# Kernel tuning notes

Hardware: AMD Instinct MI355X
Metric: run time of the kernel (lower is better)

## Reference

```python
import jax, jax.numpy as jnp
import numpy as np
from jax import lax

IMSIZE = 4096
LINEWIDTH = 31  # odd, matches torch init adjustment


def _gen_kernel(lw):
    # Nested concentric squares: layer i covers [i, lw-i) with value (i+1)/(center+1);
    # inner layers overwrite outer ones, so value = (center - chebyshev_r + 1)/(center+1).
    c = lw // 2
    idx = jnp.arange(lw)
    r = jnp.maximum(jnp.abs(idx[:, None] - c), jnp.abs(idx[None, :] - c))
    val = (c - r + 1).astype(jnp.float32) / jnp.float32(c + 1)
    return jnp.broadcast_to(val, (3, 3, lw, lw))


def _rasterize(x0, y0, x1, y1, imsize):
    # Faithful port of the torch Bresenham variant (including the inner while loop).
    # All coordinate math is non-differentiable in the original (done via .data),
    # so we stop gradients here.
    x0 = lax.stop_gradient(x0)
    y0 = lax.stop_gradient(y0)
    x1 = lax.stop_gradient(x1)
    y1 = lax.stop_gradient(y1)
    dx = jnp.abs(x1 - x0)
    dy = jnp.abs(y1 - y0)
    sx = jnp.where(x1 > x0, 1.0, -1.0)
    sy = jnp.where(y1 > y0, 1.0, -1.0)
    steep = dy > dx
    # swap (x0,y0), (dx,dy), (sx,sy) when steep
    a = jnp.where(steep, y0, x0)
    b = jnp.where(steep, x0, y0)
    dX = jnp.where(steep, dy, dx)
    dY = jnp.where(steep, dx, dy)
    sa = jnp.where(steep, sy, sx)
    sb = jnp.where(steep, sx, sy)
    d = 2.0 * dY - dX
    n = dX.astype(jnp.int32)
    mask0 = jnp.zeros((imsize, imsize), dtype=jnp.float32)

    def body(i, carry):
        a, b, d, mask = carry
        row = jnp.where(steep, b, a).astype(jnp.int32)
        col = jnp.where(steep, a, b).astype(jnp.int32)
        mask = mask.at[row, col].set(1.0)

        def inner(bd):
            bb, dd = bd
            return (bb + sb, dd - 2.0 * dX)

        b, d = lax.while_loop(lambda bd: bd[1] >= 0.0, inner, (b, d))
        a = a + sa
        d = d + 2.0 * dY
        return (a, b, d, mask)

    _, _, _, mask = lax.fori_loop(0, n, body, (a, b, d, mask0))
    mask = mask.at[x1.astype(jnp.int32), y1.astype(jnp.int32)].set(1.0)
    return mask


def setup_inputs() -> dict:
    return {
        "x0": jnp.array([100.0], dtype=jnp.float32),
        "y0": jnp.array([200.0], dtype=jnp.float32),
        "x1": jnp.array([3900.0], dtype=jnp.float32),
        "y1": jnp.array([3500.0], dtype=jnp.float32),
    }


def reference(x0, y0, x1, y1):
    imsize, lw = IMSIZE, LINEWIDTH
    mask = _rasterize(x0[0], y0[0], x1[0], y1[0], imsize)  # [H, W]
    img = jnp.broadcast_to(mask, (1, 3, imsize, imsize))   # NCHW
    kernel = _gen_kernel(lw)                               # OIHW [3,3,lw,lw]
    pad = lw // 2
    out = lax.conv_general_dilated(
        img, kernel, window_strides=(1, 1),
        padding=[(pad, pad), (pad, pad)],
        dimension_numbers=("NCHW", "OIHW", "NCHW"))
    tmin = jnp.min(out)
    tmax = jnp.max(out)
    out = (out - tmin) / (tmax - tmin)
    return 1.0 - out[0]  # [3, imsize, imsize]
```

## Files before the change

### kernel.cpp

```cpp
#include <hip/hip_runtime.h>
#include <cstdint>
#include <cstddef>

#define IMSIZE 4096
#define HALF 15
#define SENT (-100000)

__global__ __launch_bounds__(1024) void k_line(
    const float* __restrict__ x0p, const float* __restrict__ y0p,
    const float* __restrict__ x1p, const float* __restrict__ y1p,
    int* __restrict__ hdr, int* __restrict__ map)
{
    int t = threadIdx.x;
    for (int i = t; i < IMSIZE; i += 1024) map[i] = SENT;
    __syncthreads();

    float x0 = x0p[0], y0 = y0p[0], x1 = x1p[0], y1 = y1p[0];
    float dx = fabsf(x1 - x0), dy = fabsf(y1 - y0);
    float sx = (x1 > x0) ? 1.f : -1.f;
    float sy = (y1 > y0) ? 1.f : -1.f;
    bool steep = dy > dx;
    float a0 = steep ? y0 : x0;
    float b0 = steep ? x0 : y0;
    float dX = steep ? dy : dx;
    float dY = steep ? dx : dy;
    float sa = steep ? sy : sx;
    float sb = steep ? sx : sy;
    int n = (int)dX;

    if (t == 0) { hdr[0] = steep ? 1 : 0; hdr[1] = 0; }

    double twodY = 2.0 * (double)dY;
    double twodX = 2.0 * (double)dX;
    double ddX   = (double)dX;
    for (int i = t; i < n; i += 1024) {
        int ki = (int)floor((twodY * (double)i + ddX) / twodX);
        float ai = a0 + sa * (float)i;
        float bi = b0 + sb * (float)ki;
        int M  = (int)ai;
        int mn = (int)bi;
        if ((unsigned)M < IMSIZE) map[M] = mn;
    }
    if (t == 0) {
        int M  = steep ? (int)y1 : (int)x1;
        int mn = steep ? (int)x1 : (int)y1;
        if ((unsigned)M < IMSIZE) map[M] = mn;
    }
}

__device__ __forceinline__ int conv_s(int i, int j, int steep,
                                      const int* __restrict__ map)
{
    int M  = steep ? j : i;
    int mn = steep ? i : j;
    int s = 0;
    #pragma unroll
    for (int dm = -HALF; dm <= HALF; ++dm) {
        int m = M + dm;
        if ((unsigned)m < IMSIZE) {
            int c = map[m];
            int ad = abs(c - mn);
            if (ad <= HALF) s += 16 - max(ad, (dm < 0 ? -dm : dm));
        }
    }
    return s;
}

__global__ __launch_bounds__(64) void k_band(
    int* __restrict__ hdr, const int* __restrict__ map,
    int* __restrict__ lo, int* __restrict__ hi)
{
    int M = blockIdx.x;
    int t = threadIdx.x;

    int v = SENT;
    if (t < 2 * HALF + 1) {
        int m = M - HALF + t;
        if ((unsigned)m < IMSIZE) v = map[m];
    }
    int vmin = (v <= SENT / 2) ? 0x7fffffff : v;
    int vmax = (v <= SENT / 2) ? (-0x7fffffff - 1) : v;
    #pragma unroll
    for (int o = 32; o >= 1; o >>= 1) {
        vmin = min(vmin, __shfl_xor(vmin, o));
        vmax = max(vmax, __shfl_xor(vmax, o));
    }
    int L, H;
    if (vmin == 0x7fffffff) { L = 1; H = 0; }
    else { L = max(vmin - HALF, 0); H = min(vmax + HALF, IMSIZE - 1); }
    if (t == 0) { lo[M] = L; hi[M] = H; }

    int steep = hdr[0];
    int smax = 0;
    for (int j = L + t; j <= H; j += 64) {
        int row = steep ? j : M;
        int col = steep ? M : j;
        smax = max(smax, conv_s(row, col, steep, map));
    }
    #pragma unroll
    for (int o = 32; o >= 1; o >>= 1) smax = max(smax, __shfl_xor(smax, o));
    if (t == 0 && smax > 0) atomicMax(hdr + 1, smax);
}

__global__ __launch_bounds__(256) void k_fill(float4* __restrict__ out)
{
    size_t idx = (size_t)blockIdx.x * 256 + threadIdx.x;
    out[idx] = make_float4(1.f, 1.f, 1.f, 1.f);
}

__global__ __launch_bounds__(64) void k_patch(
    const int* __restrict__ hdr, const int* __restrict__ map,
    const int* __restrict__ lo, const int* __restrict__ hi,
    float* __restrict__ out)
{
    int M = blockIdx.x;
    int t = threadIdx.x;
    int L = lo[M], H = hi[M];
    int steep = hdr[0];
    float inv = 1.0f / (float)hdr[1];
    const size_t CH = (size_t)IMSIZE * IMSIZE;

    for (int j = L + t; j <= H; j += 64) {
        int row = steep ? j : M;
        int col = steep ? M : j;
        int s = conv_s(row, col, steep, map);
        float val = 1.0f - (float)s * inv;
        size_t p = (size_t)row * IMSIZE + col;
        out[p]          = val;
        out[p + CH]     = val;
        out[p + 2 * CH] = val;
    }
}

extern "C" void kernel_launch(void* const* d_in, const int* in_sizes, int n_in,
                              void* d_out, int out_size, void* d_ws, size_t ws_size,
                              hipStream_t stream)
{
    const float* x0 = (const float*)d_in[0];
    const float* y0 = (const float*)d_in[1];
    const float* x1 = (const float*)d_in[2];
    const float* y1 = (const float*)d_in[3];

    int* ws  = (int*)d_ws;
    int* hdr = ws;
    int* map = ws + 16;
    int* lo  = ws + 16 + IMSIZE;
    int* hi  = ws + 16 + 2 * IMSIZE;
    float* out = (float*)d_out;

    const int NF4 = 3 * IMSIZE * IMSIZE / 4;

    hipLaunchKernelGGL(k_fill,  dim3(NF4 / 256), dim3(256),  0, stream,
                       (float4*)out);
    hipLaunchKernelGGL(k_line,  dim3(1),         dim3(1024), 0, stream,
                       x0, y0, x1, y1, hdr, map);
    hipLaunchKernelGGL(k_band,  dim3(IMSIZE),    dim3(64),   0, stream,
                       hdr, map, lo, hi);
    hipLaunchKernelGGL(k_patch, dim3(IMSIZE),    dim3(64),   0, stream,
                       hdr, map, lo, hi, out);
}
```

Baseline: 250.7 us.

## Compute line map analytically per row, drop line/band kernels and workspace map

Removes the single-block line rasterization kernel and the global map/lo/hi arrays. Each row block now recomputes its 31-entry window of the Bresenham map analytically into shared memory and derives the band bounds itself, in both the max pass and the patch pass. The fill kernel becomes grid-stride with fewer blocks and also resets the max header. This cuts one serial launch and the global-memory round trips, at the cost of redundant per-block double-precision division work.

```diff
diff --git a/kernel.cpp b/kernel.cpp
--- a/kernel.cpp
+++ b/kernel.cpp
@@ -5,126 +5,131 @@
 #define IMSIZE 4096
 #define HALF 15
 #define SENT (-100000)
+#define INT_MAXV 0x7fffffff
+#define INT_MINV (-0x7fffffff - 1)
 
-__global__ __launch_bounds__(1024) void k_line(
+struct LineP {
+    int steep, saPos, Mbase, n, Mend, mnend;
+    float b0, sb;
+    double twodY, twodX, ddX;
+};
+
+__device__ __forceinline__ LineP line_params(
     const float* __restrict__ x0p, const float* __restrict__ y0p,
-    const float* __restrict__ x1p, const float* __restrict__ y1p,
-    int* __restrict__ hdr, int* __restrict__ map)
+    const float* __restrict__ x1p, const float* __restrict__ y1p)
 {
-    int t = threadIdx.x;
-    for (int i = t; i < IMSIZE; i += 1024) map[i] = SENT;
-    __syncthreads();
-
     float x0 = x0p[0], y0 = y0p[0], x1 = x1p[0], y1 = y1p[0];
     float dx = fabsf(x1 - x0), dy = fabsf(y1 - y0);
     float sx = (x1 > x0) ? 1.f : -1.f;
     float sy = (y1 > y0) ? 1.f : -1.f;
-    bool steep = dy > dx;
-    float a0 = steep ? y0 : x0;
-    float b0 = steep ? x0 : y0;
-    float dX = steep ? dy : dx;
-    float dY = steep ? dx : dy;
-    float sa = steep ? sy : sx;
-    float sb = steep ? sx : sy;
-    int n = (int)dX;
-
-    if (t == 0) { hdr[0] = steep ? 1 : 0; hdr[1] = 0; }
-
-    double twodY = 2.0 * (double)dY;
-    double twodX = 2.0 * (double)dX;
-    double ddX   = (double)dX;
-    for (int i = t; i < n; i += 1024) {
-        int ki = (int)floor((twodY * (double)i + ddX) / twodX);
-        float ai = a0 + sa * (float)i;
-        float bi = b0 + sb * (float)ki;
-        int M  = (int)ai;
-        int mn = (int)bi;
-        if ((unsigned)M < IMSIZE) map[M] = mn;
-    }
-    if (t == 0) {
-        int M  = steep ? (int)y1 : (int)x1;
-        int mn = steep ? (int)x1 : (int)y1;
-        if ((unsigned)M < IMSIZE) map[M] = mn;
-    }
+    LineP P;
+    P.steep = dy > dx;
+    float a0 = P.steep ? y0 : x0;
+    float dX = P.steep ? dy : dx;
+    float dY = P.steep ? dx : dy;
+    float sa = P.steep ? sy : sx;
+    P.b0 = P.steep ? x0 : y0;
+    P.sb = P.steep ? sx : sy;
+    P.saPos = sa > 0.f;
+    P.Mbase = (int)a0;
+    P.n     = (int)dX;
+    P.Mend  = P.steep ? (int)y1 : (int)x1;
+    P.mnend = P.steep ? (int)x1 : (int)y1;
+    P.twodY = 2.0 * (double)dY;
+    P.twodX = 2.0 * (double)dX;
+    P.ddX   = (double)dX;
+    return P;
 }
 
-__device__ __forceinline__ int conv_s(int i, int j, int steep,
-                                      const int* __restrict__ map)
+__device__ __forceinline__ int map_at(const LineP& P, int m)
 {
-    int M  = steep ? j : i;
-    int mn = steep ? i : j;
-    int s = 0;
-    #pragma unroll
-    for (int dm = -HALF; dm <= HALF; ++dm) {
-        int m = M + dm;
-        if ((unsigned)m < IMSIZE) {
-            int c = map[m];
-            int ad = abs(c - mn);
-            if (ad <= HALF) s += 16 - max(ad, (dm < 0 ? -dm : dm));
-        }
-    }
-    return s;
+    if ((unsigned)m >= IMSIZE) return SENT;
+    if (m == P.Mend) return P.mnend;
+    int i = P.saPos ? (m - P.Mbase) : (P.Mbase - m);
+    if (i < 0 || i >= P.n) return SENT;
+    int ki = (int)floor((P.twodY * (double)i + P.ddX) / P.twodX);
+    float bi = P.b0 + P.sb * (float)ki;
+    return (int)bi;
 }
 
-__global__ __launch_bounds__(64) void k_band(
-    int* __restrict__ hdr, const int* __restrict__ map,
-    int* __restrict__ lo, int* __restrict__ hi)
+__device__ __forceinline__ void band_window(
+    const LineP& P, int M, int t, int* wmap, int& L, int& H)
 {
-    int M = blockIdx.x;
-    int t = threadIdx.x;
-
-    int v = SENT;
-    if (t < 2 * HALF + 1) {
-        int m = M - HALF + t;
-        if ((unsigned)m < IMSIZE) v = map[m];
-    }
-    int vmin = (v <= SENT / 2) ? 0x7fffffff : v;
-    int vmax = (v <= SENT / 2) ? (-0x7fffffff - 1) : v;
+    if (t < 2 * HALF + 1) wmap[t] = map_at(P, M - HALF + t);
+    __syncthreads();
+    int v = (t < 2 * HALF + 1) ? wmap[t] : SENT;
+    int vmin = (v <= SENT / 2) ? INT_MAXV : v;
+    int vmax = (v <= SENT / 2) ? INT_MINV : v;
     #pragma unroll
     for (int o = 32; o >= 1; o >>= 1) {
         vmin = min(vmin, __shfl_xor(vmin, o));
         vmax = max(vmax, __shfl_xor(vmax, o));
     }
+    if (vmin == INT_MAXV) { L = 1; H = 0; }
+    else { L = max(vmin - HALF, 0); H = min(vmax + HALF, IMSIZE - 1); }
+}
+
+__device__ __forceinline__ int conv_w(const int* __restrict__ wmap, int j)
+{
+    int s = 0;
+    #pragma unroll
+    for (int dm = -HALF; dm <= HALF; ++dm) {
+        int c = wmap[dm + HALF];
+        int ad = abs(c - j);
+        if (ad <= HALF) s += 16 - max(ad, (dm < 0 ? -dm : dm));
+    }
+    return s;
+}
+
+__global__ __launch_bounds__(256) void k_fill(float4* __restrict__ out,
+                                              int* __restrict__ hdr)
+{
+    if (blockIdx.x == 0 && threadIdx.x == 0) hdr[1] = 0;
+    const size_t N4 = (size_t)3 * IMSIZE * IMSIZE / 4;
+    size_t stride = (size_t)gridDim.x * 256;
+    const float4 one = make_float4(1.f, 1.f, 1.f, 1.f);
+    for (size_t i = (size_t)blockIdx.x * 256 + threadIdx.x; i < N4; i += stride)
+        out[i] = one;
+}
+
+__global__ __launch_bounds__(64) void k_smax(
+    const float* __restrict__ x0p, const float* __restrict__ y0p,
+    const float* __restrict__ x1p, const float* __restrict__ y1p,
+    int* __restrict__ hdr)
+{
+    __shared__ int wmap[32];
+    LineP P = line_params(x0p, y0p, x1p, y1p);
+    int M = blockIdx.x, t = threadIdx.x;
     int L, H;
-    if (vmin == 0x7fffffff) { L = 1; H = 0; }
-    else { L = max(vmin - HALF, 0); H = min(vmax + HALF, IMSIZE - 1); }
-    if (t == 0) { lo[M] = L; hi[M] = H; }
+    band_window(P, M, t, wmap, L, H);
 
-    int steep = hdr[0];
     int smax = 0;
-    for (int j = L + t; j <= H; j += 64) {
-        int row = steep ? j : M;
-        int col = steep ? M : j;
-        smax = max(smax, conv_s(row, col, steep, map));
-    }
+    for (int j = L + t; j <= H; j += 64)
+        smax = max(smax, conv_w(wmap, j));
     #pragma unroll
     for (int o = 32; o >= 1; o >>= 1) smax = max(smax, __shfl_xor(smax, o));
-    if (t == 0 && smax > 0) atomicMax(hdr + 1, smax);
-}
-
-__global__ __launch_bounds__(256) void k_fill(float4* __restrict__ out)
-{
-    size_t idx = (size_t)blockIdx.x * 256 + threadIdx.x;
-    out[idx] = make_float4(1.f, 1.f, 1.f, 1.f);
+    if (t == 0) atomicMax(hdr + 1, smax);
 }
 
 __global__ __launch_bounds__(64) void k_patch(
-    const int* __restrict__ hdr, const int* __restrict__ map,
-    const int* __restrict__ lo, const int* __restrict__ hi,
-    float* __restrict__ out)
+    const float* __restrict__ x0p, const float* __restrict__ y0p,
+    const float* __restrict__ x1p, const float* __restrict__ y1p,
+    const int* __restrict__ hdr, float* __restrict__ out)
 {
-    int M = blockIdx.x;
-    int t = threadIdx.x;
-    int L = lo[M], H = hi[M];
-    int steep = hdr[0];
+    __shared__ int wmap[32];
+    LineP P = line_params(x0p, y0p, x1p, y1p);
+    int M = blockIdx.x, t = threadIdx.x;
+    int L, H;
+    band_window(P, M, t, wmap, L, H);
+    if (L > H) return;
+
     float inv = 1.0f / (float)hdr[1];
     const size_t CH = (size_t)IMSIZE * IMSIZE;
-
     for (int j = L + t; j <= H; j += 64) {
-        int row = steep ? j : M;
-        int col = steep ? M : j;
-        int s = conv_s(row, col, steep, map);
+        int s = conv_w(wmap, j);
         float val = 1.0f - (float)s * inv;
+        int row = P.steep ? j : M;
+        int col = P.steep ? M : j;
         size_t p = (size_t)row * IMSIZE + col;
         out[p]          = val;
         out[p + CH]     = val;
@@ -141,21 +146,13 @@
     const float* x1 = (const float*)d_in[2];
     const float* y1 = (const float*)d_in[3];
 
-    int* ws  = (int*)d_ws;
-    int* hdr = ws;
-    int* map = ws + 16;
-    int* lo  = ws + 16 + IMSIZE;
-    int* hi  = ws + 16 + 2 * IMSIZE;
+    int* hdr = (int*)d_ws;
     float* out = (float*)d_out;
 
-    const int NF4 = 3 * IMSIZE * IMSIZE / 4;
-
-    hipLaunchKernelGGL(k_fill,  dim3(NF4 / 256), dim3(256),  0, stream,
-                       (float4*)out);
-    hipLaunchKernelGGL(k_line,  dim3(1),         dim3(1024), 0, stream,
-                       x0, y0, x1, y1, hdr, map);
-    hipLaunchKernelGGL(k_band,  dim3(IMSIZE),    dim3(64),   0, stream,
-                       hdr, map, lo, hi);
-    hipLaunchKernelGGL(k_patch, dim3(IMSIZE),    dim3(64),   0, stream,
-                       hdr, map, lo, hi, out);
+    hipLaunchKernelGGL(k_fill,  dim3(2048),   dim3(256), 0, stream,
+                       (float4*)out, hdr);
+    hipLaunchKernelGGL(k_smax,  dim3(IMSIZE), dim3(64),  0, stream,
+                       x0, y0, x1, y1, hdr);
+    hipLaunchKernelGGL(k_patch, dim3(IMSIZE), dim3(64),  0, stream,
+                       x0, y0, x1, y1, hdr, out);
 }
```

After: 257.4 us. 1.03x slower.
